# Kernel optimization log

Hardware: AMD Instinct MI355X
Metric: run time of the kernel (lower is better)

## Reference

```python
import jax, jax.numpy as jnp
import numpy as np

B, T, C, N = 4, 4, 32, 16384
F_OUT = 64
K = 9          # kernel_size
DIL = 1        # dilation
PAD = 4 * DIL  # padding * dilation, as in the torch module


def _unfold1d(a, k, pad, dil):
    """im2col along the last axis. a: [..., N] -> [..., k, N] (stride 1)."""
    ap = jnp.pad(a, [(0, 0)] * (a.ndim - 1) + [(pad, pad)])
    n = a.shape[-1]
    idx = jnp.arange(k)[:, None] * dil + jnp.arange(n)[None, :]  # [k, N]
    return ap[..., idx]


def setup_inputs() -> dict:
    key = jax.random.key(0)
    k1, k2, k3 = jax.random.split(key, 3)
    x = jax.random.normal(k1, (B, T, C, N), dtype=jnp.float32)
    coords = jax.random.normal(k2, (B, T, 3, N), dtype=jnp.float32)
    weight = jax.random.normal(k3, (T, F_OUT, C, K), dtype=jnp.float32) * 0.05
    return {"x": x, "coords": coords, "weight": weight, "sigma": 2}


def reference(x, coords, weight, sigma):
    # im2col windows of features: [B, T, C, K, N]  (channel-major then kernel,
    # matching F.unfold's (C*K, L) layout)
    win = _unfold1d(x, K, PAD, DIL)
    # im2col windows of coords: [B, T, 3, K, N]
    cw = _unfold1d(coords, K, PAD, DIL)
    # subtract center tap (k = K//2)
    diff = cw - cw[:, :, :, K // 2, :][:, :, :, None, :]
    d2 = jnp.sum(diff * diff, axis=2)  # [B, T, K, N]
    # safe sqrt: forward-identical, avoids NaN grads at the zero-distance center
    d = jnp.where(d2 > 0, jnp.sqrt(jnp.where(d2 > 0, d2, 1.0)), 0.0)
    # distance weights, clamped at 0 (torch: dist_weights[dist_weights<0]=0)
    w = jnp.maximum(1.0 - d / sigma, 0.0)  # [B, T, K, N]
    # weight windows; repeat over C in torch == broadcast over C here
    win = win * w[:, :, None, :, :]  # [B, T, C, K, N]
    # batched matmul over flattened (C*K): out[b,t,f,n]
    out = jnp.einsum('btckn,tfck->btfn', win, weight)
    return out
```

## Files before the change

### kernel.cpp

```cpp
#include <hip/hip_runtime.h>
#include <math.h>

#define Bd   4
#define Td   4
#define Cd   32
#define Nd   16384
#define Fd   64
#define Kd   9
#define PADd 4
#define NT   128
#define NROWS (NT + 2*PADd)
#define NCHUNK (NROWS/4)
#define XP    40
#define EPIT  36

typedef __attribute__((ext_vector_type(8))) _Float16 half8;
typedef __attribute__((ext_vector_type(4))) float    float4v;

#define A_WS_BYTES ((size_t)Td * Kd * 4 * 64 * 8 * 2)

#define SM_XT  0
#define SM_WL  10880
#define SM_CS  15488
#define SM_BYTES 18432

union FragU { uint4 u; half8 h; };

__device__ __forceinline__ float sigma_as_float(const void* p) {
    int iv = *(const int*)p;
    if (iv > 0 && iv < 1000000) return (float)iv;
    return __int_as_float(iv);
}

__device__ __forceinline__ unsigned short f32_to_f16_bits(float f) {
    _Float16 h = (_Float16)f;
    return *reinterpret_cast<unsigned short*>(&h);
}

__global__ void prep_weights(const float* __restrict__ w, unsigned short* __restrict__ a) {
    int idx = blockIdx.x * 256 + threadIdx.x;
    if (idx >= Td * Kd * 4 * 64 * 8) return;
    int j    = idx & 7;
    int lane = (idx >> 3) & 63;
    int ft   = (idx >> 9) & 3;
    int k    = (idx >> 11) % Kd;
    int t    = idx / (Kd * 4 * 64 * 8);
    int m = lane & 15, q = lane >> 4;
    int f = ft * 16 + m;
    int c = q * 8 + j;
    float v = w[(((size_t)t * Fd + f) * Cd + c) * Kd + k];
    a[idx] = f32_to_f16_bits(v);
}

__global__ __launch_bounds__(256, 4)
void swconv_mfma4(const float* __restrict__ x,
                  const float* __restrict__ coords,
                  const unsigned short* __restrict__ aw,
                  const void* __restrict__ sigma_p,
                  float* __restrict__ out)
{
    __shared__ __align__(16) unsigned char smem[SM_BYTES];
    unsigned short (*xt)[XP] = (unsigned short (*)[XP])(smem + SM_XT);
    unsigned int (*wlp)[NT]  = (unsigned int (*)[NT])(smem + SM_WL);
    float (*cs)[NROWS]       = (float (*)[NROWS])(smem + SM_CS);

    const int tid  = threadIdx.x;
    const int lane = tid & 63;
    const int wv   = tid >> 6;
    const int tile = blockIdx.x, t = blockIdx.y, b = blockIdx.z;
    const int n0   = tile * NT;
    const float inv_sigma = 1.0f / sigma_as_float(sigma_p);

    const float* xbt = x + (size_t)(b * Td + t) * Cd * Nd;
    #pragma unroll 2
    for (int i = tid; i < Cd * NCHUNK; i += 256) {
        int c  = i / NCHUNK;
        int rq = i - c * NCHUNK;
        int nf = n0 - PADd + rq * 4;
        float4 v = make_float4(0.f, 0.f, 0.f, 0.f);
        if (nf >= 0 && nf < Nd)
            v = *reinterpret_cast<const float4*>(xbt + (size_t)c * Nd + nf);
        int r = rq * 4;
        xt[r + 0][c] = f32_to_f16_bits(v.x);
        xt[r + 1][c] = f32_to_f16_bits(v.y);
        xt[r + 2][c] = f32_to_f16_bits(v.z);
        xt[r + 3][c] = f32_to_f16_bits(v.w);
    }

    const float* cbt = coords + (size_t)(b * Td + t) * 3 * Nd;
    for (int i = tid; i < 3 * NROWS; i += 256) {
        int c = i / NROWS, r = i - c * NROWS;
        int n = n0 - PADd + r;
        cs[c][r] = (n >= 0 && n < Nd) ? cbt[(size_t)c * Nd + n] : 0.0f;
    }

    const int m = lane & 15, q = lane >> 4;
    const unsigned short* Abase = aw + (size_t)t * Kd * 4 * 64 * 8 + (size_t)lane * 8;
    FragU afr[2][4];
    #pragma unroll
    for (int ft = 0; ft < 4; ++ft)
        afr[0][ft].u = *reinterpret_cast<const uint4*>(Abase + (size_t)ft * 512);

    __syncthreads();

    {
        int nl   = wv * 32 + (lane & 31);
        int half = lane >> 5;
        int il   = nl + PADd;
        float c0 = cs[0][il], c1 = cs[1][il], c2 = cs[2][il];
        int k0 = half ? 5 : 0, k1 = half ? Kd : 5;
        #pragma unroll
        for (int k = k0; k < k1; ++k) {
            float d0 = cs[0][nl + k] - c0;
            float d1 = cs[1][nl + k] - c1;
            float d2 = cs[2][nl + k] - c2;
            float s = d0 * d0 + d1 * d1 + d2 * d2;
            float d = (s > 0.0f) ? sqrtf(s) : 0.0f;
            float w = fmaxf(1.0f - d * inv_sigma, 0.0f);
            wlp[k][nl] = (unsigned int)f32_to_f16_bits(w) * 0x00010001u;
        }
    }

    float4v acc[4][2];
    #pragma unroll
    for (int ft = 0; ft < 4; ++ft)
        #pragma unroll
        for (int nt = 0; nt < 2; ++nt)
            acc[ft][nt] = (float4v){0.f, 0.f, 0.f, 0.f};

    for (int k = 0; k < Kd; ++k) {
        const int cur = k & 1;
        if (k + 1 < Kd) {
            #pragma unroll
            for (int ft = 0; ft < 4; ++ft)
                afr[cur ^ 1][ft].u = *reinterpret_cast<const uint4*>(Abase + (size_t)((k + 1) * 4 + ft) * 512);
        }
        #pragma unroll
        for (int nt = 0; nt < 2; ++nt) {
            const int ncol = wv * 32 + nt * 16 + m;
            const int r    = ncol + k;
            FragU xv; xv.u = *reinterpret_cast<const uint4*>(&xt[r][q * 8]);
            unsigned int wp = wlp[k][ncol];
            FragU ww; ww.u = make_uint4(wp, wp, wp, wp);
            half8 bfr = xv.h * ww.h;
            #pragma unroll
            for (int ft = 0; ft < 4; ++ft)
                acc[ft][nt] = __builtin_amdgcn_mfma_f32_16x16x32_f16(afr[cur][ft].h, bfr, acc[ft][nt], 0, 0, 0);
        }
    }

    __syncthreads();
    float (*epi)[EPIT] = (float (*)[EPIT])(smem + (size_t)wv * 32 * EPIT * 4);

    float* ob = out + (size_t)(b * Td + t) * Fd * Nd + n0 + wv * 32;
    #pragma unroll
    for (int fc = 0; fc < 2; ++fc) {
        #pragma unroll
        for (int ft2 = 0; ft2 < 2; ++ft2) {
            const int ft = fc * 2 + ft2;
            #pragma unroll
            for (int nt = 0; nt < 2; ++nt) {
                const int np = nt * 16 + m;
                #pragma unroll
                for (int rr = 0; rr < 4; ++rr)
                    epi[ft2 * 16 + q * 4 + rr][np] = acc[ft][nt][rr];
            }
        }
        #pragma unroll
        for (int inst = 0; inst < 4; ++inst) {
            const int fl = inst * 8 + (lane >> 3);
            const int np = (lane & 7) * 4;
            float4 v = *reinterpret_cast<const float4*>(&epi[fl][np]);
            *reinterpret_cast<float4*>(ob + (size_t)(fc * 32 + fl) * Nd + np) = v;
        }
    }
}

__global__ __launch_bounds__(256, 4)
void swconv_f32_kernel(const float* __restrict__ x,
                       const float* __restrict__ coords,
                       const float* __restrict__ weight,
                       const void*  __restrict__ sigma_p,
                       float* __restrict__ out)
{
    __shared__ float xsf[Cd][NROWS + 1];
    __shared__ float csf[3][NROWS + 1];
    const int tid = threadIdx.x;
    const int tile = blockIdx.x, t = blockIdx.y, b = blockIdx.z;
    const int n0 = tile * NT;
    const float inv_sigma = 1.0f / sigma_as_float(sigma_p);

    const float* xbt = x + (size_t)(b * Td + t) * Cd * Nd;
    for (int idx = tid; idx < Cd * NROWS; idx += 256) {
        int c = idx / NROWS, i = idx - c * NROWS, n = n0 - PADd + i;
        xsf[c][i] = (n >= 0 && n < Nd) ? xbt[(size_t)c * Nd + n] : 0.0f;
    }
    const float* cbt = coords + (size_t)(b * Td + t) * 3 * Nd;
    for (int idx = tid; idx < 3 * NROWS; idx += 256) {
        int c = idx / NROWS, i = idx - c * NROWS, n = n0 - PADd + i;
        csf[c][i] = (n >= 0 && n < Nd) ? cbt[(size_t)c * Nd + n] : 0.0f;
    }
    __syncthreads();
    if (tid >= NT) return;

    float wk[Kd];
    {
        const float c0 = csf[0][tid + PADd], c1 = csf[1][tid + PADd], c2 = csf[2][tid + PADd];
        #pragma unroll
        for (int k = 0; k < Kd; ++k) {
            float d0 = csf[0][tid + k] - c0, d1 = csf[1][tid + k] - c1, d2 = csf[2][tid + k] - c2;
            float s = d0 * d0 + d1 * d1 + d2 * d2;
            float d = (s > 0.0f) ? sqrtf(s) : 0.0f;
            wk[k] = fmaxf(1.0f - d * inv_sigma, 0.0f);
        }
    }
    float accf[Fd];
    #pragma unroll
    for (int f = 0; f < Fd; ++f) accf[f] = 0.0f;
    const float* wt = weight + (size_t)t * Fd * Cd * Kd;
    for (int c = 0; c < Cd; ++c) {
        float xv[Kd];
        #pragma unroll
        for (int k = 0; k < Kd; ++k) xv[k] = xsf[c][tid + k];
        const float* wp = wt + c * Kd;
        #pragma unroll
        for (int k = 0; k < Kd; ++k) {
            float v = xv[k] * wk[k];
            #pragma unroll
            for (int f = 0; f < Fd; ++f)
                accf[f] = fmaf(v, wp[(size_t)f * Cd * Kd + k], accf[f]);
        }
    }
    float* op = out + (size_t)(b * Td + t) * Fd * Nd + n0 + tid;
    #pragma unroll
    for (int f = 0; f < Fd; ++f) op[(size_t)f * Nd] = accf[f];
}

extern "C" void kernel_launch(void* const* d_in, const int* in_sizes, int n_in,
                              void* d_out, int out_size, void* d_ws, size_t ws_size,
                              hipStream_t stream) {
    const float* x      = (const float*)d_in[0];
    const float* coords = (const float*)d_in[1];
    const float* weight = (const float*)d_in[2];
    const void*  sigma  = d_in[3];
    float* out = (float*)d_out;

    if (ws_size >= A_WS_BYTES) {
        unsigned short* aw = (unsigned short*)d_ws;
        prep_weights<<<(Td * Kd * 4 * 64 * 8 + 255) / 256, 256, 0, stream>>>(weight, aw);
        dim3 grid(Nd / NT, Td, Bd);
        swconv_mfma4<<<grid, dim3(256), 0, stream>>>(x, coords, aw, sigma, out);
    } else {
        dim3 grid(Nd / NT, Td, Bd);
        swconv_f32_kernel<<<grid, dim3(256), 0, stream>>>(x, coords, weight, sigma, out);
    }
}
```

Before: 111.0 us.

## Swizzle fp16 feature tile in LDS, pack loads, use nontemporal output stores

The x staging loop is rewritten so each thread loads four channels at the same position with coalesced scalar reads, packs them into fp16 pairs and writes 8-byte chunks into an XOR-swizzled LDS layout. The MFMA B-fragment read applies the matching swizzle, aiming to cut LDS bank conflicts from the old 2-byte scattered stores. Weight prep now packs two fp16 values per 32-bit write, and output stores become nontemporal to avoid polluting cache. The new scalar global loads issue more instructions than the float4 loads they replace.

```diff
diff --git a/kernel.cpp b/kernel.cpp
--- a/kernel.cpp
+++ b/kernel.cpp
@@ -10,12 +10,12 @@
 #define PADd 4
 #define NT   128
 #define NROWS (NT + 2*PADd)
-#define NCHUNK (NROWS/4)
 #define XP    40
 #define EPIT  36
 
 typedef __attribute__((ext_vector_type(8))) _Float16 half8;
 typedef __attribute__((ext_vector_type(4))) float    float4v;
+typedef __attribute__((ext_vector_type(4))) float    f32x4;
 
 #define A_WS_BYTES ((size_t)Td * Kd * 4 * 64 * 8 * 2)
 
@@ -37,19 +37,28 @@
     return *reinterpret_cast<unsigned short*>(&h);
 }
 
-__global__ void prep_weights(const float* __restrict__ w, unsigned short* __restrict__ a) {
+__device__ __forceinline__ unsigned int pack_f16x2(float a, float b) {
+    unsigned int lo = f32_to_f16_bits(a);
+    unsigned int hi = f32_to_f16_bits(b);
+    return lo | (hi << 16);
+}
+
+__global__ void prep_weights(const float* __restrict__ w, unsigned int* __restrict__ a) {
     int idx = blockIdx.x * 256 + threadIdx.x;
-    if (idx >= Td * Kd * 4 * 64 * 8) return;
-    int j    = idx & 7;
-    int lane = (idx >> 3) & 63;
-    int ft   = (idx >> 9) & 3;
-    int k    = (idx >> 11) % Kd;
-    int t    = idx / (Kd * 4 * 64 * 8);
+    if (idx >= Td * Kd * 4 * 64 * 4) return;
+    int jp   = idx & 3;
+    int lane = (idx >> 2) & 63;
+    int ft   = (idx >> 8) & 3;
+    int tk   = idx >> 10;
+    int k    = tk % Kd;
+    int t    = tk / Kd;
     int m = lane & 15, q = lane >> 4;
     int f = ft * 16 + m;
-    int c = q * 8 + j;
-    float v = w[(((size_t)t * Fd + f) * Cd + c) * Kd + k];
-    a[idx] = f32_to_f16_bits(v);
+    int c = q * 8 + jp * 2;
+    const float* wp = w + (((size_t)t * Fd + f) * Cd + c) * Kd + k;
+    float v0 = wp[0];
+    float v1 = wp[Kd];
+    a[idx] = pack_f16x2(v0, v1);
 }
 
 __global__ __launch_bounds__(256, 4)
@@ -60,7 +69,6 @@
                   float* __restrict__ out)
 {
     __shared__ __align__(16) unsigned char smem[SM_BYTES];
-    unsigned short (*xt)[XP] = (unsigned short (*)[XP])(smem + SM_XT);
     unsigned int (*wlp)[NT]  = (unsigned int (*)[NT])(smem + SM_WL);
     float (*cs)[NROWS]       = (float (*)[NROWS])(smem + SM_CS);
 
@@ -72,19 +80,30 @@
     const float inv_sigma = 1.0f / sigma_as_float(sigma_p);
 
     const float* xbt = x + (size_t)(b * Td + t) * Cd * Nd;
-    #pragma unroll 2
-    for (int i = tid; i < Cd * NCHUNK; i += 256) {
-        int c  = i / NCHUNK;
-        int rq = i - c * NCHUNK;
-        int nf = n0 - PADd + rq * 4;
-        float4 v = make_float4(0.f, 0.f, 0.f, 0.f);
-        if (nf >= 0 && nf < Nd)
-            v = *reinterpret_cast<const float4*>(xbt + (size_t)c * Nd + nf);
-        int r = rq * 4;
-        xt[r + 0][c] = f32_to_f16_bits(v.x);
-        xt[r + 1][c] = f32_to_f16_bits(v.y);
-        xt[r + 2][c] = f32_to_f16_bits(v.z);
-        xt[r + 3][c] = f32_to_f16_bits(v.w);
+    #pragma unroll
+    for (int half = 0; half < 2; ++half) {
+        const int cg = wv * 2 + half;
+        const float* xc = xbt + (size_t)(cg * 4) * Nd;
+        #pragma unroll
+        for (int rr = 0; rr < 3; ++rr) {
+            int r = rr * 64 + lane;
+            if (r < NROWS) {
+                int n = n0 - PADd + r;
+                float v0 = 0.f, v1 = 0.f, v2 = 0.f, v3 = 0.f;
+                if (n >= 0 && n < Nd) {
+                    v0 = xc[n];
+                    v1 = xc[n + Nd];
+                    v2 = xc[n + 2 * Nd];
+                    v3 = xc[n + 3 * Nd];
+                }
+                unsigned int p0 = pack_f16x2(v0, v1);
+                unsigned int p1 = pack_f16x2(v2, v3);
+                int chunk = (cg >> 1) ^ ((r >> 3) & 3);
+                unsigned char* dst = smem + SM_XT + (size_t)r * (XP * 2)
+                                   + chunk * 16 + (cg & 1) * 8;
+                *reinterpret_cast<uint2*>(dst) = make_uint2(p0, p1);
+            }
+        }
     }
 
     const float* cbt = coords + (size_t)(b * Td + t) * 3 * Nd;
@@ -105,10 +124,10 @@
 
     {
         int nl   = wv * 32 + (lane & 31);
-        int half = lane >> 5;
+        int hf   = lane >> 5;
         int il   = nl + PADd;
         float c0 = cs[0][il], c1 = cs[1][il], c2 = cs[2][il];
-        int k0 = half ? 5 : 0, k1 = half ? Kd : 5;
+        int k0 = hf ? 5 : 0, k1 = hf ? Kd : 5;
         #pragma unroll
         for (int k = k0; k < k1; ++k) {
             float d0 = cs[0][nl + k] - c0;
@@ -139,7 +158,9 @@
         for (int nt = 0; nt < 2; ++nt) {
             const int ncol = wv * 32 + nt * 16 + m;
             const int r    = ncol + k;
-            FragU xv; xv.u = *reinterpret_cast<const uint4*>(&xt[r][q * 8]);
+            const int ch   = q ^ ((r >> 3) & 3);
+            FragU xv;
+            xv.u = *reinterpret_cast<const uint4*>(smem + SM_XT + (size_t)r * (XP * 2) + ch * 16);
             unsigned int wp = wlp[k][ncol];
             FragU ww; ww.u = make_uint4(wp, wp, wp, wp);
             half8 bfr = xv.h * ww.h;
@@ -170,8 +191,8 @@
         for (int inst = 0; inst < 4; ++inst) {
             const int fl = inst * 8 + (lane >> 3);
             const int np = (lane & 7) * 4;
-            float4 v = *reinterpret_cast<const float4*>(&epi[fl][np]);
-            *reinterpret_cast<float4*>(ob + (size_t)(fc * 32 + fl) * Nd + np) = v;
+            f32x4 v = *reinterpret_cast<const f32x4*>(&epi[fl][np]);
+            __builtin_nontemporal_store(v, reinterpret_cast<f32x4*>(ob + (size_t)(fc * 32 + fl) * Nd + np));
         }
     }
 }
@@ -246,10 +267,10 @@
     float* out = (float*)d_out;
 
     if (ws_size >= A_WS_BYTES) {
-        unsigned short* aw = (unsigned short*)d_ws;
-        prep_weights<<<(Td * Kd * 4 * 64 * 8 + 255) / 256, 256, 0, stream>>>(weight, aw);
+        unsigned int* aw = (unsigned int*)d_ws;
+        prep_weights<<<(Td * Kd * 4 * 64 * 4 + 255) / 256, 256, 0, stream>>>(weight, aw);
         dim3 grid(Nd / NT, Td, Bd);
-        swconv_mfma4<<<grid, dim3(256), 0, stream>>>(x, coords, aw, sigma, out);
+        swconv_mfma4<<<grid, dim3(256), 0, stream>>>(x, coords, (const unsigned short*)aw, sigma, out);
     } else {
         dim3 grid(Nd / NT, Td, Bd);
         swconv_f32_kernel<<<grid, dim3(256), 0, stream>>>(x, coords, weight, sigma, out);
```

Measured after the change: 119.4 us. 1.08x slower.
